# Kernel optimization log

Measured on AMD Instinct MI355X. Metric: run time of the kernel, lower is better.

Reference implementation:

```python
import jax, jax.numpy as jnp
import numpy as np
import math

D_MODEL = 512
N_HEAD = 8
D_HEAD = 64
N_LAYER = 12
D_FF = 2048
EMB_SIZES = [32, 128, 256, 256, 32, 64]
N_TOKEN = [32, 32, 90, 70, 8, 8]
EPS_ATTN = 1e-6
EPS_LN = 1e-5


def _pos_encoding(seq, d):
    pos = np.arange(seq, dtype=np.float32)[:, None]
    div = np.exp(np.arange(0, d, 2, dtype=np.float32) * (-math.log(10000.0) / d))
    pe = np.zeros((seq, d), np.float32)
    pe[:, 0::2] = np.sin(pos * div)
    pe[:, 1::2] = np.cos(pos * div)
    return jnp.asarray(pe)


def _layernorm(x, g, b):
    mu = jnp.mean(x, axis=-1, keepdims=True)
    var = jnp.var(x, axis=-1, keepdims=True)
    return (x - mu) * jax.lax.rsqrt(var + EPS_LN) * g + b


def _phi(x):
    # elu(x) + 1
    return jnp.where(x > 0, x + 1.0, jnp.exp(x))


def _causal_linear_attention(h, wq, bq, wk, bk, wv, bv, wo, bo):
    B, S, _ = h.shape
    q = _phi((h @ wq + bq).reshape(B, S, N_HEAD, D_HEAD))
    k = _phi((h @ wk + bk).reshape(B, S, N_HEAD, D_HEAD))
    v = (h @ wv + bv).reshape(B, S, N_HEAD, D_HEAD)
    # cumulative K^T V state: [B,S,H,D,D]
    kv = jnp.cumsum(k[..., :, None] * v[..., None, :], axis=1)
    ksum = jnp.cumsum(k, axis=1)
    z = 1.0 / (jnp.einsum('bshd,bshd->bsh', q, ksum) + EPS_ATTN)
    out = jnp.einsum('bshd,bshde->bshe', q, kv) * z[..., None]
    return out.reshape(B, S, D_MODEL) @ wo + bo


def _forward(x, emb_bar, emb_position, emb_pitch, emb_duration, emb_type, emb_emotion,
             in_w, in_b, wq, bq, wk, bk, wv, bv, wo, bo,
             ln1_g, ln1_b, w1, b1, w2, b2, ln2_g, ln2_b,
             lnf_g, lnf_b, proj_emo_w, proj_emo_b):
    tables = [emb_bar, emb_position, emb_pitch, emb_duration, emb_type, emb_emotion]
    embs = jnp.concatenate(
        [jnp.take(t, x[..., i], axis=0) * math.sqrt(EMB_SIZES[i]) for i, t in enumerate(tables)],
        axis=-1)  # [B,S,768]
    h = embs @ in_w + in_b
    S = h.shape[1]
    h = h + _pos_encoding(S, D_MODEL)[None, :, :]  # dropout is identity in eval

    def layer(hc, p):
        (wq_, bq_, wk_, bk_, wv_, bv_, wo_, bo_,
         g1, be1, w1_, b1_, w2_, b2_, g2, be2) = p
        hc = hc + _causal_linear_attention(hc, wq_, bq_, wk_, bk_, wv_, bv_, wo_, bo_)
        hc = _layernorm(hc, g1, be1)
        y = jax.nn.gelu(hc @ w1_ + b1_, approximate=False) @ w2_ + b2_
        hc = _layernorm(hc + y, g2, be2)
        return hc, None

    params = (wq, bq, wk, bk, wv, bv, wo, bo, ln1_g, ln1_b, w1, b1, w2, b2, ln2_g, ln2_b)
    h, _ = jax.lax.scan(layer, h, params)
    h = _layernorm(h, lnf_g, lnf_b)  # final encoder norm
    y_emotion = h @ proj_emo_w + proj_emo_b
    return h, y_emotion


def setup_inputs() -> dict:
    key = jax.random.key(0)
    ks = jax.random.split(key, 16)
    B, S = 1, 1024
    x = jax.random.randint(ks[0], (B, S, 6), 0, 8)

    def lin(k, fin, fout):
        k1, k2 = jax.random.split(k)
        lim = 1.0 / np.sqrt(fin)
        return (jax.random.uniform(k1, (fin, fout), minval=-lim, maxval=lim),
                jax.random.uniform(k2, (fout,), minval=-lim, maxval=lim))

    def stack_lin(k, fin, fout):
        kk = jax.random.split(k, N_LAYER)
        ws, bs = zip(*[lin(kk[i], fin, fout) for i in range(N_LAYER)])
        return jnp.stack(ws), jnp.stack(bs)

    def stack_ln(val):
        return jnp.full((N_LAYER, D_MODEL), val, jnp.float32)

    inp = {'x': x}
    names = ['emb_bar', 'emb_position', 'emb_pitch', 'emb_duration', 'emb_type', 'emb_emotion']
    for i, n in enumerate(names):
        inp[n] = jax.random.normal(jax.random.fold_in(ks[1], i), (N_TOKEN[i], EMB_SIZES[i])) * 0.02
    inp['in_w'], inp['in_b'] = lin(ks[2], sum(EMB_SIZES), D_MODEL)
    inp['wq'], inp['bq'] = stack_lin(ks[3], D_MODEL, D_MODEL)
    inp['wk'], inp['bk'] = stack_lin(ks[4], D_MODEL, D_MODEL)
    inp['wv'], inp['bv'] = stack_lin(ks[5], D_MODEL, D_MODEL)
    inp['wo'], inp['bo'] = stack_lin(ks[6], D_MODEL, D_MODEL)
    inp['ln1_g'], inp['ln1_b'] = stack_ln(1.0), stack_ln(0.0)
    inp['w1'], inp['b1'] = stack_lin(ks[7], D_MODEL, D_FF)
    inp['w2'], inp['b2'] = stack_lin(ks[8], D_FF, D_MODEL)
    inp['ln2_g'], inp['ln2_b'] = stack_ln(1.0), stack_ln(0.0)
    inp['lnf_g'], inp['lnf_b'] = jnp.ones((D_MODEL,)), jnp.zeros((D_MODEL,))
    inp['proj_emo_w'], inp['proj_emo_b'] = lin(ks[9], D_MODEL, N_TOKEN[5])
    return inp


def reference(x, emb_bar, emb_position, emb_pitch, emb_duration, emb_type, emb_emotion,
              in_w, in_b, wq, bq, wk, bk, wv, bv, wo, bo,
              ln1_g, ln1_b, w1, b1, w2, b2, ln2_g, ln2_b,
              lnf_g, lnf_b, proj_emo_w, proj_emo_b):
    return _forward(x, emb_bar, emb_position, emb_pitch, emb_duration, emb_type, emb_emotion,
                    in_w, in_b, wq, bq, wk, bk, wv, bv, wo, bo,
                    ln1_g, ln1_b, w1, b1, w2, b2, ln2_g, ln2_b,
                    lnf_g, lnf_b, proj_emo_w, proj_emo_b)
```

## Files before the change

kernel.cpp:

```cpp
#include <hip/hip_runtime.h>
#include <hip/hip_bf16.h>
#include <math.h>


#define S_LEN 1024
#define DM 512
#define NH 8
#define DH 64
#define DFF 2048
#define NLAYER 12
#define CHUNK 64
#define NCH (S_LEN / CHUNK)

#define ACT_NONE 0
#define ACT_PHI  1
#define ACT_GELU 2

typedef short s16x8 __attribute__((ext_vector_type(8)));
typedef float f32x4 __attribute__((ext_vector_type(4)));

__device__ __forceinline__ short f2bf(float x) {
    __hip_bfloat16 h = __float2bfloat16(x);
    return *reinterpret_cast<short*>(&h);
}

__device__ __forceinline__ void fma4(f32x4& a, float s, const f32x4 v) {
    a.x = fmaf(s, v.x, a.x); a.y = fmaf(s, v.y, a.y);
    a.z = fmaf(s, v.z, a.z); a.w = fmaf(s, v.w, a.w);
}

__device__ __forceinline__ void tile_barrier() {
    asm volatile("s_waitcnt lgkmcnt(0)" ::: "memory");
    __builtin_amdgcn_s_barrier();
    asm volatile("" ::: "memory");
}

__global__ __launch_bounds__(256) void embed_kernel(
    const int* __restrict__ x,
    const float* __restrict__ t0, const float* __restrict__ t1,
    const float* __restrict__ t2, const float* __restrict__ t3,
    const float* __restrict__ t4, const float* __restrict__ t5,
    short* __restrict__ EMBb)
{
    int s = blockIdx.x;
    __shared__ int xi[6];
    if (threadIdx.x < 6) xi[threadIdx.x] = x[s * 6 + threadIdx.x];
    __syncthreads();
    for (int j = threadIdx.x; j < 768; j += 256) {
        int i, off, width; const float* t; float sc;
        if (j < 32)       { i = 0; off = 0;   t = t0; sc = 5.656854249f;  width = 32;  }
        else if (j < 160) { i = 1; off = 32;  t = t1; sc = 11.3137085f;   width = 128; }
        else if (j < 416) { i = 2; off = 160; t = t2; sc = 16.0f;         width = 256; }
        else if (j < 672) { i = 3; off = 416; t = t3; sc = 16.0f;         width = 256; }
        else if (j < 704) { i = 4; off = 672; t = t4; sc = 5.656854249f;  width = 32;  }
        else              { i = 5; off = 704; t = t5; sc = 8.0f;          width = 64;  }
        EMBb[s * 768 + j] = f2bf(t[xi[i] * width + (j - off)] * sc);
    }
}

__global__ __launch_bounds__(256) void transpose_w(
    const float* __restrict__ in, short* __restrict__ out, int K, int N)
{
    __shared__ short t[64][66];
    const int b = blockIdx.z;
    const int n0 = blockIdx.x * 64, k0 = blockIdx.y * 64;
    const float* ip = in + (size_t)b * K * N;
    short* op = out + (size_t)b * K * N;
    const int c = threadIdx.x & 63, r0 = (threadIdx.x >> 6) * 16;
    #pragma unroll
    for (int i = 0; i < 16; ++i)
        t[c][r0 + i] = f2bf(ip[(size_t)(k0 + r0 + i) * N + n0 + c]);
    __syncthreads();
    #pragma unroll
    for (int i = 0; i < 16; ++i)
        op[(size_t)(n0 + r0 + i) * K + k0 + c] = t[r0 + i][c];
}

__global__ __launch_bounds__(256) void transpose4_w(
    const float* __restrict__ wA, const float* __restrict__ wB,
    const float* __restrict__ wC, const float* __restrict__ wD,
    short* __restrict__ oA, short* __restrict__ oB,
    short* __restrict__ oC, short* __restrict__ oD)
{
    __shared__ short t[64][66];
    const int zz = blockIdx.z;
    const int which = zz & 3, b = zz >> 2;
    const float* in = (which == 0) ? wA : (which == 1) ? wB : (which == 2) ? wC : wD;
    short* out      = (which == 0) ? oA : (which == 1) ? oB : (which == 2) ? oC : oD;
    const int n0 = blockIdx.x * 64, k0 = blockIdx.y * 64;
    const float* ip = in + (size_t)b * DM * DM;
    short* op = out + (size_t)b * DM * DM;
    const int c = threadIdx.x & 63, r0 = (threadIdx.x >> 6) * 16;
    #pragma unroll
    for (int i = 0; i < 16; ++i)
        t[c][r0 + i] = f2bf(ip[(size_t)(k0 + r0 + i) * DM + n0 + c]);
    __syncthreads();
    #pragma unroll
    for (int i = 0; i < 16; ++i)
        op[(size_t)(n0 + r0 + i) * DM + k0 + c] = t[r0 + i][c];
}

__device__ __forceinline__ float apply_act(float v, int act) {
    if (act == ACT_PHI)       return (v > 0.0f) ? (v + 1.0f) : expf(v);
    else if (act == ACT_GELU) return 0.5f * v * (1.0f + erff(v * 0.70710678118654752f));
    return v;
}


__device__ __forceinline__ void ldswr64(short* lds, int srow, int scolb,
                                        const s16x8 r[2])
{
    const int bc = scolb ^ ((srow & 7) << 4);
    #pragma unroll
    for (int p = 0; p < 2; ++p)
        *(s16x8*)((char*)lds + (p * 32 + srow) * 128 + bc) = r[p];
}

__device__ __forceinline__ void compute64(
    const short* __restrict__ As, const short* __restrict__ Bs,
    int wr, int wc, int l15, int q, f32x4 acc[2][2])
{
    #pragma unroll
    for (int kh = 0; kh < 2; ++kh) {
        const int kb = kh * 64 + q * 16;
        s16x8 a[2], b[2];
        #pragma unroll
        for (int m = 0; m < 2; ++m) {
            int row = wr * 32 + m * 16 + l15;
            a[m] = *(const s16x8*)((const char*)As + row * 128 + (kb ^ ((row & 7) << 4)));
        }
        #pragma unroll
        for (int n = 0; n < 2; ++n) {
            int row = wc * 32 + n * 16 + l15;
            b[n] = *(const s16x8*)((const char*)Bs + row * 128 + (kb ^ ((row & 7) << 4)));
        }
        #pragma unroll
        for (int m = 0; m < 2; ++m)
            #pragma unroll
            for (int n = 0; n < 2; ++n)
                acc[m][n] = __builtin_amdgcn_mfma_f32_16x16x32_bf16(
                    a[m], b[n], acc[m][n], 0, 0, 0);
    }
}

__device__ __forceinline__ void compute64x2(
    const short* __restrict__ As, const short* __restrict__ Bs0,
    const short* __restrict__ Bs1,
    int wr, int wc, int l15, int q, f32x4 acc0[2][2], f32x4 acc1[2][2])
{
    #pragma unroll
    for (int kh = 0; kh < 2; ++kh) {
        const int kb = kh * 64 + q * 16;
        s16x8 a[2], b0[2], b1[2];
        #pragma unroll
        for (int m = 0; m < 2; ++m) {
            int row = wr * 32 + m * 16 + l15;
            a[m] = *(const s16x8*)((const char*)As + row * 128 + (kb ^ ((row & 7) << 4)));
        }
        #pragma unroll
        for (int n = 0; n < 2; ++n) {
            int row = wc * 32 + n * 16 + l15;
            int off = row * 128 + (kb ^ ((row & 7) << 4));
            b0[n] = *(const s16x8*)((const char*)Bs0 + off);
            b1[n] = *(const s16x8*)((const char*)Bs1 + off);
        }
        #pragma unroll
        for (int m = 0; m < 2; ++m)
            #pragma unroll
            for (int n = 0; n < 2; ++n) {
                acc0[m][n] = __builtin_amdgcn_mfma_f32_16x16x32_bf16(
                    a[m], b0[n], acc0[m][n], 0, 0, 0);
                acc1[m][n] = __builtin_amdgcn_mfma_f32_16x16x32_bf16(
                    a[m], b1[n], acc1[m][n], 0, 0, 0);
            }
    }
}

__global__ __launch_bounds__(256) void gemm64(
    const short* __restrict__ A, const short* __restrict__ BT,
    const float* __restrict__ bias, const float* __restrict__ resid,
    float* __restrict__ Cf, short* __restrict__ Cbf,
    int N, int K, int act, int add_pe, int zparts)
{
    __shared__ short As[2][4096];
    __shared__ short Bs[2][4096];
    const int tid = threadIdx.x;
    const int row0 = blockIdx.y * 64, col0 = blockIdx.x * 64;
    const int z = blockIdx.z;
    const int Kz = K / zparts;
    const int kbase = z * Kz;
    const int w = tid >> 6, lane = tid & 63, q = lane >> 4, l15 = lane & 15;
    const int wr = w >> 1, wc = w & 1;
    const int nt = Kz >> 6;

    const int srow = tid >> 3;
    const int scolb = (tid & 7) * 16;
    const char* gA = (const char*)(A  + (size_t)(row0 + srow) * K + kbase) + scolb;
    const char* gB = (const char*)(BT + (size_t)(col0 + srow) * K + kbase) + scolb;
    const size_t rstep = (size_t)32 * K * 2;

    s16x8 ra[2], rb[2];
    #pragma unroll
    for (int p = 0; p < 2; ++p) {
        ra[p] = *(const s16x8*)(gA + p * rstep);
        rb[p] = *(const s16x8*)(gB + p * rstep);
    }
    ldswr64(As[0], srow, scolb, ra);
    ldswr64(Bs[0], srow, scolb, rb);
    if (nt > 1) {
        #pragma unroll
        for (int p = 0; p < 2; ++p) {
            ra[p] = *(const s16x8*)(gA + p * rstep + 128);
            rb[p] = *(const s16x8*)(gB + p * rstep + 128);
        }
    }
    tile_barrier();

    f32x4 acc[2][2] = {};
    int cur = 0;
    for (int t = 0; t < nt; ++t) {
        compute64(As[cur], Bs[cur], wr, wc, l15, q, acc);
        if (t + 1 < nt) {
            ldswr64(As[cur ^ 1], srow, scolb, ra);
            ldswr64(Bs[cur ^ 1], srow, scolb, rb);
            if (t + 2 < nt) {
                size_t ko = (size_t)(t + 2) * 128;
                #pragma unroll
                for (int p = 0; p < 2; ++p) {
                    ra[p] = *(const s16x8*)(gA + p * rstep + ko);
                    rb[p] = *(const s16x8*)(gB + p * rstep + ko);
                }
            }
            tile_barrier();
        }
        cur ^= 1;
    }

    if (zparts > 1 && Cf) Cf += (size_t)z * S_LEN * N;

    const int rbase = row0 + wr * 32 + q * 4;
    const int cbase = col0 + wc * 32 + l15;
    #pragma unroll
    for (int n = 0; n < 2; ++n) {
        int c = cbase + n * 16;
        float bia = (z == 0) ? bias[c] : 0.0f;
        #pragma unroll
        for (int m = 0; m < 2; ++m) {
            #pragma unroll
            for (int rg = 0; rg < 4; ++rg) {
                int r = rbase + m * 16 + rg;
                float v = apply_act(acc[m][n][rg] + bia, act);
                if (resid) v += resid[(size_t)r * N + c];
                if (add_pe) {
                    float freq = expf((float)(c & ~1) * (-9.210340371976184f / 512.0f));
                    float ang = (float)r * freq;
                    v += (c & 1) ? cosf(ang) : sinf(ang);
                }
                if (Cf)  Cf[(size_t)r * N + c] = v;
                if (Cbf) Cbf[(size_t)r * N + c] = f2bf(v);
            }
        }
    }
}

__global__ __launch_bounds__(256) void qkv_fused(
    const short* __restrict__ Hb,
    const short* __restrict__ qT, const short* __restrict__ kT, const short* __restrict__ vT,
    const float* __restrict__ bq, const float* __restrict__ bk, const float* __restrict__ bv,
    float* __restrict__ Qb, float* __restrict__ Kb, float* __restrict__ Vb,
    float* __restrict__ KVC, float* __restrict__ KSC)
{
    __shared__ char smem[49152];
    short* As  = (short*)smem;
    short* Bs0 = (short*)(smem + 16384);
    short* Bs1 = (short*)(smem + 32768);

    const int tid = threadIdx.x;
    const bool isKV = blockIdx.x >= 8;
    const int colb = blockIdx.x & 7;
    const int col0 = colb * 64;
    const int row0 = blockIdx.y * 64;
    const int w = tid >> 6, lane = tid & 63, q = lane >> 4, l15 = lane & 15;
    const int wr = w >> 1, wc = w & 1;

    const int srow = tid >> 3;
    const int scolb = (tid & 7) * 16;
    const char* gA = (const char*)(Hb + (size_t)(row0 + srow) * DM) + scolb;
    const size_t rstep = (size_t)32 * DM * 2;

    if (!isKV) {
        const char* gB = (const char*)(qT + (size_t)(col0 + srow) * DM) + scolb;
        s16x8 ra[2], rb[2];
        #pragma unroll
        for (int p = 0; p < 2; ++p) {
            ra[p] = *(const s16x8*)(gA + p * rstep);
            rb[p] = *(const s16x8*)(gB + p * rstep);
        }
        ldswr64(As, srow, scolb, ra);
        ldswr64(Bs0, srow, scolb, rb);
        #pragma unroll
        for (int p = 0; p < 2; ++p) {
            ra[p] = *(const s16x8*)(gA + p * rstep + 128);
            rb[p] = *(const s16x8*)(gB + p * rstep + 128);
        }
        tile_barrier();

        f32x4 acc[2][2] = {};
        int cur = 0;
        for (int t = 0; t < 8; ++t) {
            compute64(As + cur * 4096, Bs0 + cur * 4096, wr, wc, l15, q, acc);
            if (t + 1 < 8) {
                ldswr64(As + (cur ^ 1) * 4096, srow, scolb, ra);
                ldswr64(Bs0 + (cur ^ 1) * 4096, srow, scolb, rb);
                if (t + 2 < 8) {
                    size_t ko = (size_t)(t + 2) * 128;
                    #pragma unroll
                    for (int p = 0; p < 2; ++p) {
                        ra[p] = *(const s16x8*)(gA + p * rstep + ko);
                        rb[p] = *(const s16x8*)(gB + p * rstep + ko);
                    }
                }
                tile_barrier();
            }
            cur ^= 1;
        }

        const int rbase = row0 + wr * 32 + q * 4;
        const int cbase = col0 + wc * 32 + l15;
        #pragma unroll
        for (int n = 0; n < 2; ++n) {
            int c = cbase + n * 16;
            float bia = bq[c];
            #pragma unroll
            for (int m = 0; m < 2; ++m) {
                #pragma unroll
                for (int rg = 0; rg < 4; ++rg) {
                    int r = rbase + m * 16 + rg;
                    float v = acc[m][n][rg] + bia;
                    v = (v > 0.0f) ? (v + 1.0f) : expf(v);
                    Qb[(size_t)r * DM + c] = v;
                }
            }
        }
        return;
    }

    const char* gBk = (const char*)(kT + (size_t)(col0 + srow) * DM) + scolb;
    const char* gBv = (const char*)(vT + (size_t)(col0 + srow) * DM) + scolb;
    s16x8 ra[2], rbk[2], rbv[2];
    #pragma unroll
    for (int p = 0; p < 2; ++p) {
        ra[p]  = *(const s16x8*)(gA + p * rstep);
        rbk[p] = *(const s16x8*)(gBk + p * rstep);
        rbv[p] = *(const s16x8*)(gBv + p * rstep);
    }
    ldswr64(As, srow, scolb, ra);
    ldswr64(Bs0, srow, scolb, rbk);
    ldswr64(Bs1, srow, scolb, rbv);
    #pragma unroll
    for (int p = 0; p < 2; ++p) {
        ra[p]  = *(const s16x8*)(gA + p * rstep + 128);
        rbk[p] = *(const s16x8*)(gBk + p * rstep + 128);
        rbv[p] = *(const s16x8*)(gBv + p * rstep + 128);
    }
    tile_barrier();

    f32x4 acck[2][2] = {}, accv[2][2] = {};
    int cur = 0;
    for (int t = 0; t < 8; ++t) {
        compute64x2(As + cur * 4096, Bs0 + cur * 4096, Bs1 + cur * 4096,
                    wr, wc, l15, q, acck, accv);
        if (t + 1 < 8) {
            ldswr64(As + (cur ^ 1) * 4096, srow, scolb, ra);
            ldswr64(Bs0 + (cur ^ 1) * 4096, srow, scolb, rbk);
            ldswr64(Bs1 + (cur ^ 1) * 4096, srow, scolb, rbv);
            if (t + 2 < 8) {
                size_t ko = (size_t)(t + 2) * 128;
                #pragma unroll
                for (int p = 0; p < 2; ++p) {
                    ra[p]  = *(const s16x8*)(gA + p * rstep + ko);
                    rbk[p] = *(const s16x8*)(gBk + p * rstep + ko);
                    rbv[p] = *(const s16x8*)(gBv + p * rstep + ko);
                }
            }
            tile_barrier();
        }
        cur ^= 1;
    }

    __syncthreads();
    float* Ksf = (float*)smem;
    float* Vsf = (float*)(smem + 17408);
    {
        const int lrb = wr * 32 + q * 4;
        const int lcb = wc * 32 + l15;
        #pragma unroll
        for (int n = 0; n < 2; ++n) {
            int lc = lcb + n * 16;
            int c = col0 + lc;
            float bk_ = bk[c], bv_ = bv[c];
            #pragma unroll
            for (int m = 0; m < 2; ++m) {
                #pragma unroll
                for (int rg = 0; rg < 4; ++rg) {
                    int lr = lrb + m * 16 + rg;
                    int r = row0 + lr;
                    float kv = acck[m][n][rg] + bk_;
                    kv = (kv > 0.0f) ? (kv + 1.0f) : expf(kv);
                    float vv = accv[m][n][rg] + bv_;
                    Kb[(size_t)r * DM + c] = kv;
                    Vb[(size_t)r * DM + c] = vv;
                    Ksf[lr * 68 + lc] = kv;
                    Vsf[lr * 68 + lc] = vv;
                }
            }
        }
    }
    __syncthreads();

    const int c = blockIdx.y, h = colb;
    const int di = (tid >> 4) * 4, ei = (tid & 15) * 4;
    f32x4 a0 = {}, a1 = {}, a2 = {}, a3 = {}, ks = {};
    #pragma unroll 8
    for (int t = 0; t < 64; ++t) {
        f32x4 kk = *(const f32x4*)(Ksf + t * 68 + di);
        f32x4 vv = *(const f32x4*)(Vsf + t * 68 + ei);
        fma4(a0, kk.x, vv); fma4(a1, kk.y, vv);
        fma4(a2, kk.z, vv); fma4(a3, kk.w, vv);
        ks += kk;
    }
    float* out = KVC + (size_t)(c * NH + h) * 4096;
    *(f32x4*)(out + (size_t)(di + 0) * 64 + ei) = a0;
    *(f32x4*)(out + (size_t)(di + 1) * 64 + ei) = a1;
    *(f32x4*)(out + (size_t)(di + 2) * 64 + ei) = a2;
    *(f32x4*)(out + (size_t)(di + 3) * 64 + ei) = a3;
    if ((tid & 15) == 0)
        *(f32x4*)(KSC + (size_t)(c * NH + h) * 64 + di) = ks;
}

__global__ __launch_bounds__(256) void attn_out_kernel(
    const float* __restrict__ Qb, const float* __restrict__ Kb,
    const float* __restrict__ Vb, const float* __restrict__ KVC,
    const float* __restrict__ KSC, short* __restrict__ Ab)
{
    const int h = blockIdx.x >> 4, c = blockIdx.x & 15;
    const int tid = threadIdx.x;
    __shared__ float Qt[64][68];
    __shared__ float Kt[64][68];
    __shared__ float Vs[64][68];
    __shared__ float Ms[64][68];
    __shared__ float St[64][68];
    __shared__ float KSs[64];

    {
        f32x4 macc[4] = {};
        for (int cp = 0; cp < c; ++cp) {
            const float* src = KVC + (size_t)(cp * NH + h) * 4096;
            #pragma unroll
            for (int it = 0; it < 4; ++it)
                macc[it] += *(const f32x4*)(src + (size_t)(tid + it * 256) * 4);
        }
        #pragma unroll
        for (int it = 0; it < 4; ++it) {
            int j = tid + it * 256;
            *(f32x4*)(&Ms[j >> 4][(j & 15) * 4]) = macc[it];
        }
        if (tid < 64) {
            float s = 0.0f;
            for (int cp = 0; cp < c; ++cp)
                s += KSC[(size_t)(cp * NH + h) * 64 + tid];
            KSs[tid] = s;
        }
    }
    #pragma unroll
    for (int it = 0; it < 4; ++it) {
        int j = tid + it * 256;
        int r = j >> 4, d0 = (j & 15) * 4;
        size_t g = (size_t)(c * CHUNK + r) * DM + h * 64 + d0;
        f32x4 q = *(const f32x4*)(Qb + g);
        f32x4 k = *(const f32x4*)(Kb + g);
        f32x4 v = *(const f32x4*)(Vb + g);
        Qt[d0 + 0][r] = q.x; Qt[d0 + 1][r] = q.y; Qt[d0 + 2][r] = q.z; Qt[d0 + 3][r] = q.w;
        Kt[d0 + 0][r] = k.x; Kt[d0 + 1][r] = k.y; Kt[d0 + 2][r] = k.z; Kt[d0 + 3][r] = k.w;
        *(f32x4*)(&Vs[r][d0]) = v;
    }
    __syncthreads();

    const int si = tid >> 4, ti = tid & 15;
    const int s0 = si * 4, t0 = ti * 4;

    f32x4 accO0 = {}, accO1 = {}, accO2 = {}, accO3 = {};
    f32x4 den = {};
    #pragma unroll 8
    for (int d = 0; d < 64; ++d) {
        f32x4 qv = *(const f32x4*)(&Qt[d][s0]);
        f32x4 mv = *(const f32x4*)(&Ms[d][t0]);
        float ks = KSs[d];
        fma4(accO0, qv.x, mv); fma4(accO1, qv.y, mv);
        fma4(accO2, qv.z, mv); fma4(accO3, qv.w, mv);
        fma4(den, ks, qv);
    }

    f32x4 p0 = {}, p1 = {}, p2 = {}, p3 = {};
    if (ti <= si) {
        #pragma unroll 8
        for (int d = 0; d < 64; ++d) {
            f32x4 qv = *(const f32x4*)(&Qt[d][s0]);
            f32x4 kv = *(const f32x4*)(&Kt[d][t0]);
            fma4(p0, qv.x, kv); fma4(p1, qv.y, kv);
            fma4(p2, qv.z, kv); fma4(p3, qv.w, kv);
        }
        if (ti == si) {
            p0.y = 0.0f; p0.z = 0.0f; p0.w = 0.0f;
            p1.z = 0.0f; p1.w = 0.0f;
            p2.w = 0.0f;
        }
    }
    St[t0 + 0][s0 + 0] = p0.x; St[t0 + 1][s0 + 0] = p0.y;
    St[t0 + 2][s0 + 0] = p0.z; St[t0 + 3][s0 + 0] = p0.w;
    St[t0 + 0][s0 + 1] = p1.x; St[t0 + 1][s0 + 1] = p1.y;
    St[t0 + 2][s0 + 1] = p1.z; St[t0 + 3][s0 + 1] = p1.w;
    St[t0 + 0][s0 + 2] = p2.x; St[t0 + 1][s0 + 2] = p2.y;
    St[t0 + 2][s0 + 2] = p2.z; St[t0 + 3][s0 + 2] = p2.w;
    St[t0 + 0][s0 + 3] = p3.x; St[t0 + 1][s0 + 3] = p3.y;
    St[t0 + 2][s0 + 3] = p3.z; St[t0 + 3][s0 + 3] = p3.w;
    __syncthreads();

    const int tmax = s0 + 4;
    #pragma unroll 4
    for (int t2 = 0; t2 < tmax; ++t2) {
        f32x4 sv = *(const f32x4*)(&St[t2][s0]);
        f32x4 vv = *(const f32x4*)(&Vs[t2][t0]);
        fma4(accO0, sv.x, vv); fma4(accO1, sv.y, vv);
        fma4(accO2, sv.z, vv); fma4(accO3, sv.w, vv);
        den += sv;
    }

    short* op = Ab + (size_t)(c * CHUNK + s0) * DM + h * 64 + t0;
    {
        float z = 1.0f / (den.x + 1e-6f);
        short4 o; o.x = f2bf(accO0.x * z); o.y = f2bf(accO0.y * z);
        o.z = f2bf(accO0.z * z); o.w = f2bf(accO0.w * z);
        *reinterpret_cast<short4*>(op) = o;
    }
    {
        float z = 1.0f / (den.y + 1e-6f);
        short4 o; o.x = f2bf(accO1.x * z); o.y = f2bf(accO1.y * z);
        o.z = f2bf(accO1.z * z); o.w = f2bf(accO1.w * z);
        *reinterpret_cast<short4*>(op + DM) = o;
    }
    {
        float z = 1.0f / (den.z + 1e-6f);
        short4 o; o.x = f2bf(accO2.x * z); o.y = f2bf(accO2.y * z);
        o.z = f2bf(accO2.z * z); o.w = f2bf(accO2.w * z);
        *reinterpret_cast<short4*>(op + 2 * DM) = o;
    }
    {
        float z = 1.0f / (den.w + 1e-6f);
        short4 o; o.x = f2bf(accO3.x * z); o.y = f2bf(accO3.y * z);
        o.z = f2bf(accO3.z * z); o.w = f2bf(accO3.w * z);
        *reinterpret_cast<short4*>(op + 3 * DM) = o;
    }
}

__global__ __launch_bounds__(64) void ln_kernel64(
    const float* __restrict__ X, const float* __restrict__ X2,
    const float* __restrict__ resid,
    const float* __restrict__ g, const float* __restrict__ b,
    float* __restrict__ O, short* __restrict__ Ob)
{
    const int row = blockIdx.x;
    const size_t base = (size_t)row * DM;
    const int t = threadIdx.x;
    const int i0 = 4 * t, i1 = 256 + 4 * t;
    f32x4 v0 = *(const f32x4*)(X + base + i0);
    f32x4 v1 = *(const f32x4*)(X + base + i1);
    if (X2) {
        v0 += *(const f32x4*)(X2 + base + i0);
        v1 += *(const f32x4*)(X2 + base + i1);
    }
    if (resid) {
        v0 += *(const f32x4*)(resid + base + i0);
        v1 += *(const f32x4*)(resid + base + i1);
    }
    float s = v0.x + v0.y + v0.z + v0.w + v1.x + v1.y + v1.z + v1.w;
    #pragma unroll
    for (int m = 1; m < 64; m <<= 1) s += __shfl_xor(s, m, 64);
    float mean = s * (1.0f / 512.0f);
    f32x4 d0 = v0 - mean, d1 = v1 - mean;
    float ss = d0.x * d0.x + d0.y * d0.y + d0.z * d0.z + d0.w * d0.w
             + d1.x * d1.x + d1.y * d1.y + d1.z * d1.z + d1.w * d1.w;
    #pragma unroll
    for (int m = 1; m < 64; m <<= 1) ss += __shfl_xor(ss, m, 64);
    float var = ss * (1.0f / 512.0f);
    float rs = 1.0f / sqrtf(var + 1e-5f);
    f32x4 g0 = *(const f32x4*)(g + i0), g1v = *(const f32x4*)(g + i1);
    f32x4 b0 = *(const f32x4*)(b + i0), b1v = *(const f32x4*)(b + i1);
    f32x4 o0 = d0 * rs * g0 + b0;
    f32x4 o1 = d1 * rs * g1v + b1v;
    *(f32x4*)(O + base + i0) = o0;
    *(f32x4*)(O + base + i1) = o1;
    if (Ob) {
        short4 s0; s0.x = f2bf(o0.x); s0.y = f2bf(o0.y); s0.z = f2bf(o0.z); s0.w = f2bf(o0.w);
        short4 s1; s1.x = f2bf(o1.x); s1.y = f2bf(o1.y); s1.z = f2bf(o1.z); s1.w = f2bf(o1.w);
        *reinterpret_cast<short4*>(Ob + base + i0) = s0;
        *reinterpret_cast<short4*>(Ob + base + i1) = s1;
    }
}

__global__ __launch_bounds__(64) void ln_final_proj(
    const float* __restrict__ X,
    const float* __restrict__ g, const float* __restrict__ b,
    const float* __restrict__ pw, const float* __restrict__ pb,
    float* __restrict__ Hout, float* __restrict__ Eout)
{
    __shared__ float hrow[512];
    const int row = blockIdx.x;
    const size_t base = (size_t)row * DM;
    const int t = threadIdx.x;
    const int i0 = 4 * t, i1 = 256 + 4 * t;
    f32x4 v0 = *(const f32x4*)(X + base + i0);
    f32x4 v1 = *(const f32x4*)(X + base + i1);
    float s = v0.x + v0.y + v0.z + v0.w + v1.x + v1.y + v1.z + v1.w;
    #pragma unroll
    for (int m = 1; m < 64; m <<= 1) s += __shfl_xor(s, m, 64);
    float mean = s * (1.0f / 512.0f);
    f32x4 d0 = v0 - mean, d1 = v1 - mean;
    float ss = d0.x * d0.x + d0.y * d0.y + d0.z * d0.z + d0.w * d0.w
             + d1.x * d1.x + d1.y * d1.y + d1.z * d1.z + d1.w * d1.w;
    #pragma unroll
    for (int m = 1; m < 64; m <<= 1) ss += __shfl_xor(ss, m, 64);
    float var = ss * (1.0f / 512.0f);
    float rs = 1.0f / sqrtf(var + 1e-5f);
    f32x4 g0 = *(const f32x4*)(g + i0), g1v = *(const f32x4*)(g + i1);
    f32x4 b0 = *(const f32x4*)(b + i0), b1v = *(const f32x4*)(b + i1);
    f32x4 o0 = d0 * rs * g0 + b0;
    f32x4 o1 = d1 * rs * g1v + b1v;
    *(f32x4*)(Hout + base + i0) = o0;
    *(f32x4*)(Hout + base + i1) = o1;
    *(f32x4*)(&hrow[i0]) = o0;
    *(f32x4*)(&hrow[i1]) = o1;
    __syncthreads();

    const int e = t & 7, seg = t >> 3;
    float acc = 0.0f;
    #pragma unroll 16
    for (int d = seg * 64; d < seg * 64 + 64; ++d)
        acc = fmaf(hrow[d], pw[d * 8 + e], acc);
    acc += __shfl_xor(acc, 8, 64);
    acc += __shfl_xor(acc, 16, 64);
    acc += __shfl_xor(acc, 32, 64);
    if (t < 8) Eout[(size_t)row * 8 + t] = acc + pb[t];
}

extern "C" void kernel_launch(void* const* d_in, const int* in_sizes, int n_in,
                              void* d_out, int out_size, void* d_ws, size_t ws_size,
                              hipStream_t stream)
{
    const int*   x    = (const int*)d_in[0];
    const float* e0   = (const float*)d_in[1];
    const float* e1   = (const float*)d_in[2];
    const float* e2   = (const float*)d_in[3];
    const float* e3   = (const float*)d_in[4];
    const float* e4   = (const float*)d_in[5];
    const float* e5   = (const float*)d_in[6];
    const float* in_w = (const float*)d_in[7];
    const float* in_b = (const float*)d_in[8];
    const float* wq   = (const float*)d_in[9];
    const float* bq   = (const float*)d_in[10];
    const float* wk   = (const float*)d_in[11];
    const float* bk   = (const float*)d_in[12];
    const float* wv   = (const float*)d_in[13];
    const float* bv   = (const float*)d_in[14];
    const float* wo   = (const float*)d_in[15];
    const float* bo   = (const float*)d_in[16];
    const float* g1   = (const float*)d_in[17];
    const float* be1  = (const float*)d_in[18];
    const float* w1   = (const float*)d_in[19];
    const float* b1   = (const float*)d_in[20];
    const float* w2   = (const float*)d_in[21];
    const float* b2   = (const float*)d_in[22];
    const float* g2   = (const float*)d_in[23];
    const float* be2  = (const float*)d_in[24];
    const float* gf   = (const float*)d_in[25];
    const float* bfin = (const float*)d_in[26];
    const float* pw   = (const float*)d_in[27];
    const float* pb   = (const float*)d_in[28];
    float* outp = (float*)d_out;

    float* ws = (float*)d_ws;
    float* H    = ws;
    float* Y    = ws + 524288;
    float* Y2   = ws + 1048576;
    float* Qb   = ws + 1572864;
    float* Kb   = ws + 2097152;
    float* Vb   = ws + 2621440;
    float* KVC  = ws + 3145728;
    float* KSC  = ws + 3670016;
    short* sb   = (short*)(ws + 3678208);
    short* Hb   = sb;
    short* Ab   = sb + 524288;
    short* FFb  = sb + 1048576;
    short* EMBb = FFb;
    short* inT  = sb + 3145728;
    short* qT   = inT + 393216;
    short* kT   = qT + 3145728;
    short* vT   = kT + 3145728;
    short* oT   = vT + 3145728;
    short* w1T  = oT + 3145728;
    short* w2T  = w1T + 12582912;

    const dim3 blk256(256), blk64(64);

    transpose_w<<<dim3(8, 12, 1),  blk256, 0, stream>>>(in_w, inT, 768, DM);
    transpose4_w<<<dim3(8, 8, 48), blk256, 0, stream>>>(wq, wk, wv, wo,
                                                        qT, kT, vT, oT);
    transpose_w<<<dim3(32, 8, 12), blk256, 0, stream>>>(w1, w1T, DM, DFF);
    transpose_w<<<dim3(8, 32, 12), blk256, 0, stream>>>(w2, w2T, DFF, DM);

    embed_kernel<<<S_LEN, blk256, 0, stream>>>(x, e0, e1, e2, e3, e4, e5, EMBb);
    gemm64<<<dim3(8, 16, 1), blk256, 0, stream>>>(EMBb, inT, in_b, nullptr,
                                                  H, Hb, DM, 768, ACT_NONE, 1, 1);

    for (int l = 0; l < NLAYER; ++l) {
        const short* qT_l = qT + (size_t)l * DM * DM;
        const short* kT_l = kT + (size_t)l * DM * DM;
        const short* vT_l = vT + (size_t)l * DM * DM;
        const short* oT_l = oT + (size_t)l * DM * DM;
        const short* w1T_l = w1T + (size_t)l * DM * DFF;
        const short* w2T_l = w2T + (size_t)l * DM * DFF;
        const float* bq_l = bq + l * DM;  const float* bk_l = bk + l * DM;
        const float* bv_l = bv + l * DM;  const float* bo_l = bo + l * DM;
        const float* b1_l = b1 + l * DFF; const float* b2_l = b2 + l * DM;

        qkv_fused<<<dim3(16, 16), blk256, 0, stream>>>(Hb, qT_l, kT_l, vT_l,
                                                       bq_l, bk_l, bv_l,
                                                       Qb, Kb, Vb, KVC, KSC);

        attn_out_kernel<<<NCH * NH, blk256, 0, stream>>>(Qb, Kb, Vb, KVC, KSC, Ab);

        gemm64<<<dim3(8, 16, 2), blk256, 0, stream>>>(Ab, oT_l, bo_l, nullptr,
                                                      Y, nullptr, DM, DM, ACT_NONE, 0, 2);
        ln_kernel64<<<S_LEN, blk64, 0, stream>>>(Y, Y2, H,
                                                 g1 + l * DM, be1 + l * DM, H, Hb);

        gemm64<<<dim3(32, 16, 1), blk256, 0, stream>>>(Hb, w1T_l, b1_l, nullptr,
                                                       nullptr, FFb, DFF, DM, ACT_GELU, 0, 1);
        gemm64<<<dim3(8, 16, 2), blk256, 0, stream>>>(FFb, w2T_l, b2_l, nullptr,
                                                      Y, nullptr, DM, DFF, ACT_NONE, 0, 2);
        ln_kernel64<<<S_LEN, blk64, 0, stream>>>(Y, Y2, H,
                                                 g2 + l * DM, be2 + l * DM, H, Hb);
    }

    ln_final_proj<<<S_LEN, blk64, 0, stream>>>(H, gf, bfin, pw, pb,
                                               outp, outp + 524288);
}
```

Baseline: 1.015 ms.

## Split GEMM K-loop across two wave groups with in-block LDS reduction

The 64x64 GEMM tile kernel now runs 512 threads: two groups of four waves each process half of the K range into separate LDS slabs, then the second group writes its accumulators to shared memory and the first adds them before the epilogue. This is meant to raise the number of waves per output tile and shorten the serial K loop for these small-grid GEMMs, which underfill the GPU. In exchange it uses 64KB of LDS per block, adds two block-wide barriers and a reduction, and leaves each group with a shorter pipeline whose prologue costs more relative to the loop. The tile_barrier inside the loop also now spans 512 threads.

```diff
diff --git a/kernel.cpp b/kernel.cpp
--- a/kernel.cpp
+++ b/kernel.cpp
@@ -176,37 +176,40 @@
     }
 }
 
-__global__ __launch_bounds__(256) void gemm64(
+__global__ __launch_bounds__(512) void gemm64x8(
     const short* __restrict__ A, const short* __restrict__ BT,
     const float* __restrict__ bias, const float* __restrict__ resid,
     float* __restrict__ Cf, short* __restrict__ Cbf,
     int N, int K, int act, int add_pe, int zparts)
 {
-    __shared__ short As[2][4096];
-    __shared__ short Bs[2][4096];
+    __shared__ char smem[65536];
     const int tid = threadIdx.x;
+    const int kg = tid >> 8, sg = tid & 255;
     const int row0 = blockIdx.y * 64, col0 = blockIdx.x * 64;
     const int z = blockIdx.z;
     const int Kz = K / zparts;
-    const int kbase = z * Kz;
-    const int w = tid >> 6, lane = tid & 63, q = lane >> 4, l15 = lane & 15;
+    const int kbase = z * Kz + kg * (Kz >> 1);
+    const int w = sg >> 6, lane = tid & 63, q = lane >> 4, l15 = lane & 15;
     const int wr = w >> 1, wc = w & 1;
-    const int nt = Kz >> 6;
-
-    const int srow = tid >> 3;
-    const int scolb = (tid & 7) * 16;
+    const int nt = Kz >> 7;
+
+    const int srow = sg >> 3;
+    const int scolb = (sg & 7) * 16;
     const char* gA = (const char*)(A  + (size_t)(row0 + srow) * K + kbase) + scolb;
     const char* gB = (const char*)(BT + (size_t)(col0 + srow) * K + kbase) + scolb;
     const size_t rstep = (size_t)32 * K * 2;
 
+    short* Aslab = (short*)(smem + kg * 16384);
+    short* Bslab = (short*)(smem + 32768 + kg * 16384);
+
     s16x8 ra[2], rb[2];
     #pragma unroll
     for (int p = 0; p < 2; ++p) {
         ra[p] = *(const s16x8*)(gA + p * rstep);
         rb[p] = *(const s16x8*)(gB + p * rstep);
     }
-    ldswr64(As[0], srow, scolb, ra);
-    ldswr64(Bs[0], srow, scolb, rb);
+    ldswr64(Aslab, srow, scolb, ra);
+    ldswr64(Bslab, srow, scolb, rb);
     if (nt > 1) {
         #pragma unroll
         for (int p = 0; p < 2; ++p) {
@@ -219,10 +222,10 @@
     f32x4 acc[2][2] = {};
     int cur = 0;
     for (int t = 0; t < nt; ++t) {
-        compute64(As[cur], Bs[cur], wr, wc, l15, q, acc);
+        compute64(Aslab + cur * 4096, Bslab + cur * 4096, wr, wc, l15, q, acc);
         if (t + 1 < nt) {
-            ldswr64(As[cur ^ 1], srow, scolb, ra);
-            ldswr64(Bs[cur ^ 1], srow, scolb, rb);
+            ldswr64(Aslab + (cur ^ 1) * 4096, srow, scolb, ra);
+            ldswr64(Bslab + (cur ^ 1) * 4096, srow, scolb, rb);
             if (t + 2 < nt) {
                 size_t ko = (size_t)(t + 2) * 128;
                 #pragma unroll
@@ -234,6 +237,28 @@
             tile_barrier();
         }
         cur ^= 1;
+    }
+
+    __syncthreads();
+    float* scratch = (float*)smem;
+    if (kg == 1) {
+        float* s = scratch + sg * 16;
+        #pragma unroll
+        for (int m = 0; m < 2; ++m)
+            #pragma unroll
+            for (int n = 0; n < 2; ++n)
+                *(f32x4*)(s + (m * 2 + n) * 4) = acc[m][n];
+    }
+    __syncthreads();
+    if (kg == 1) return;
+
+    {
+        float* s = scratch + sg * 16;
+        #pragma unroll
+        for (int m = 0; m < 2; ++m)
+            #pragma unroll
+            for (int n = 0; n < 2; ++n)
+                acc[m][n] += *(const f32x4*)(s + (m * 2 + n) * 4);
     }
 
     if (zparts > 1 && Cf) Cf += (size_t)z * S_LEN * N;
@@ -710,7 +735,7 @@
     short* w1T  = oT + 3145728;
     short* w2T  = w1T + 12582912;
 
-    const dim3 blk256(256), blk64(64);
+    const dim3 blk256(256), blk64(64), blk512(512);
 
     transpose_w<<<dim3(8, 12, 1),  blk256, 0, stream>>>(in_w, inT, 768, DM);
     transpose4_w<<<dim3(8, 8, 48), blk256, 0, stream>>>(wq, wk, wv, wo,
@@ -719,8 +744,8 @@
     transpose_w<<<dim3(8, 32, 12), blk256, 0, stream>>>(w2, w2T, DFF, DM);
 
     embed_kernel<<<S_LEN, blk256, 0, stream>>>(x, e0, e1, e2, e3, e4, e5, EMBb);
-    gemm64<<<dim3(8, 16, 1), blk256, 0, stream>>>(EMBb, inT, in_b, nullptr,
-                                                  H, Hb, DM, 768, ACT_NONE, 1, 1);
+    gemm64x8<<<dim3(8, 16, 1), blk512, 0, stream>>>(EMBb, inT, in_b, nullptr,
+                                                    H, Hb, DM, 768, ACT_NONE, 1, 1);
 
     for (int l = 0; l < NLAYER; ++l) {
         const short* qT_l = qT + (size_t)l * DM * DM;
@@ -739,15 +764,15 @@
 
         attn_out_kernel<<<NCH * NH, blk256, 0, stream>>>(Qb, Kb, Vb, KVC, KSC, Ab);
 
-        gemm64<<<dim3(8, 16, 2), blk256, 0, stream>>>(Ab, oT_l, bo_l, nullptr,
-                                                      Y, nullptr, DM, DM, ACT_NONE, 0, 2);
+        gemm64x8<<<dim3(8, 16, 2), blk512, 0, stream>>>(Ab, oT_l, bo_l, nullptr,
+                                                        Y, nullptr, DM, DM, ACT_NONE, 0, 2);
         ln_kernel64<<<S_LEN, blk64, 0, stream>>>(Y, Y2, H,
                                                  g1 + l * DM, be1 + l * DM, H, Hb);
 
-        gemm64<<<dim3(32, 16, 1), blk256, 0, stream>>>(Hb, w1T_l, b1_l, nullptr,
-                                                       nullptr, FFb, DFF, DM, ACT_GELU, 0, 1);
-        gemm64<<<dim3(8, 16, 2), blk256, 0, stream>>>(FFb, w2T_l, b2_l, nullptr,
-                                                      Y, nullptr, DM, DFF, ACT_NONE, 0, 2);
+        gemm64x8<<<dim3(32, 16, 1), blk512, 0, stream>>>(Hb, w1T_l, b1_l, nullptr,
+                                                         nullptr, FFb, DFF, DM, ACT_GELU, 0, 1);
+        gemm64x8<<<dim3(8, 16, 2), blk512, 0, stream>>>(FFb, w2T_l, b2_l, nullptr,
+                                                        Y, nullptr, DM, DFF, ACT_NONE, 0, 2);
         ln_kernel64<<<S_LEN, blk64, 0, stream>>>(Y, Y2, H,
                                                  g2 + l * DM, be2 + l * DM, H, Hb);
     }
```

New measurement: 998.6 us. No clear change (-1.6%).
